# Optimization experiments

Measured on AMD Instinct MI355X. Metric: run time of the kernel, lower is better.

## Reference

```python
import jax, jax.numpy as jnp
import numpy as np

EPS = 1e-8  # torch cosine_similarity eps


def setup_inputs() -> dict:
    key = jax.random.key(0)
    ks = jax.random.split(key, 8)
    B, D = 65536, 1024
    s = lambda fi, fo: (1.0 / np.sqrt(fi))
    return {
        "image_features": jax.random.normal(ks[0], (B, D), jnp.float32),
        "W1": jax.random.normal(ks[1], (D, 512), jnp.float32) * s(D, 512),
        "b1": jnp.zeros((512,), jnp.float32),
        "W2": jax.random.normal(ks[2], (512, 256), jnp.float32) * s(512, 256),
        "b2": jnp.zeros((256,), jnp.float32),
        "W3": jax.random.normal(ks[3], (256, 128), jnp.float32) * s(256, 128),
        "b3": jnp.zeros((128,), jnp.float32),
        "emb": jax.random.normal(ks[4], (1000, 128), jnp.float32),
    }


def reference(image_features, W1, b1, W2, b2, W3, b3, emb):
    # MLP projection (dropout is identity at inference)
    h = jax.nn.relu(image_features @ W1 + b1)
    h = jax.nn.relu(h @ W2 + b2)
    proj = h @ W3 + b3                              # [B, 128]
    # cosine similarity against all 1000 scene embeddings, fused as
    # normalize + small matmul instead of the broadcasted [B,1000,128] tensor
    pn = proj / jnp.maximum(jnp.linalg.norm(proj, axis=-1, keepdims=True), EPS)
    en = emb / jnp.maximum(jnp.linalg.norm(emb, axis=-1, keepdims=True), EPS)
    sims = pn @ en.T                                # [B, 1000]
    top_indices = jnp.argmax(sims, axis=1)          # [B]
    return top_indices
```

## Files before the change

kernel.cpp:

```cpp
#include <hip/hip_runtime.h>
#include <math.h>

#define EPS 1e-8f
#define TAU 1e-4f

typedef _Float16 half_t;
typedef __attribute__((ext_vector_type(8))) _Float16 f16x8;
typedef __attribute__((ext_vector_type(4))) float f32x4;

__device__ __forceinline__ void gload16(const half_t* g, half_t* l) {
    __builtin_amdgcn_global_load_lds((const __attribute__((address_space(1))) void*)g,
                                     (__attribute__((address_space(3))) void*)l, 16, 0, 0);
}

__device__ __forceinline__ void split2(float a, half_t& h, half_t& l) {
    h = (half_t)a;
    l = (half_t)(a - (float)h);
}


__global__ __launch_bounds__(64) void emb_norm_kernel(const float* __restrict__ emb,
                                                      float* __restrict__ enT) {
    const int row = blockIdx.x;
    const int t = threadIdx.x;
    float e0 = emb[row * 128 + t];
    float e1 = emb[row * 128 + 64 + t];
    float s = e0 * e0 + e1 * e1;
#pragma unroll
    for (int off = 32; off >= 1; off >>= 1) s += __shfl_xor(s, off);
    float denom = fmaxf(sqrtf(s), EPS);
    enT[(size_t)t * 1000 + row]        = e0 / denom;
    enT[(size_t)(64 + t) * 1000 + row] = e1 / denom;
}

__global__ __launch_bounds__(64) void emb_split_kernel(const float* __restrict__ emb,
                                                       half_t* __restrict__ eTh,
                                                       half_t* __restrict__ eTl) {
    const int n = blockIdx.x;
    const int t = threadIdx.x;
    float e0 = 0.f, e1 = 0.f;
    if (n < 1000) {
        e0 = emb[n * 128 + t];
        e1 = emb[n * 128 + 64 + t];
    }
    float s = e0 * e0 + e1 * e1;
#pragma unroll
    for (int off = 32; off >= 1; off >>= 1) s += __shfl_xor(s, off);
    float denom = fmaxf(sqrtf(s), EPS);
    float v0 = (n < 1000) ? e0 / denom : 0.f;
    float v1 = (n < 1000) ? e1 / denom : 0.f;
    half_t h, l;
    int f0 = t, f1 = 64 + t;
    size_t p0 = ((size_t)(f0 >> 3) * 1024 + n) * 8 + (f0 & 7);
    size_t p1 = ((size_t)(f1 >> 3) * 1024 + n) * 8 + (f1 & 7);
    split2(v0, h, l); eTh[p0] = h; eTl[p0] = l;
    split2(v1, h, l); eTh[p1] = h; eTl[p1] = l;
}

template<int N>
__global__ __launch_bounds__(256) void wsplit_kernel(const float* __restrict__ W,
                                                     half_t* __restrict__ Wh,
                                                     half_t* __restrict__ Wl) {
    int idx = blockIdx.x * 256 + threadIdx.x;
    int k = idx / N, n = idx % N;
    float w = W[idx];
    half_t h, l;
    split2(w, h, l);
    size_t pos = ((size_t)(k >> 3) * N + n) * 8 + (k & 7);
    Wh[pos] = h; Wl[pos] = l;
}

#define EPI_RELU 0
#define EPI_NORM 1

template<int K, int N, bool AF32, int EPI>
__global__ __launch_bounds__(256, 2) void gemm16(
    const float* __restrict__ A32,
    const half_t* __restrict__ Agh, const half_t* __restrict__ Agl,
    const half_t* __restrict__ Bgh, const half_t* __restrict__ Bgl,
    const float* __restrict__ bias,
    half_t* __restrict__ Oh, half_t* __restrict__ Ol)
{
    __shared__ alignas(16) half_t sAh[8][128][8];
    __shared__ alignas(16) half_t sAl[8][128][8];
    __shared__ alignas(16) half_t sBh[8][128][8];
    __shared__ alignas(16) half_t sBl[8][128][8];

    const int t = threadIdx.x;
    const int lane = t & 63, w = t >> 6;
    const int lr = lane & 15, lg = lane >> 4;
    const int wm = w >> 1, wn = w & 1;

    const int nwg = gridDim.x * gridDim.y;
    const int lin = blockIdx.x + gridDim.x * blockIdx.y;
    const int cpx = nwg >> 3;
    const int logical = (lin & 7) * cpx + (lin >> 3);
    const int bx = logical % gridDim.x;
    const int by = logical / gridDim.x;
    const int m0 = by * 128, n0 = bx * 128;

    f32x4 acc[4][4] = {};

    for (int k0 = 0; k0 < K; k0 += 64) {
        if constexpr (AF32) {
#pragma unroll
            for (int q = 0; q < 4; ++q) {
                int s = t + 256 * q;
                int row = s >> 3, kb = s & 7;
                const float* src = A32 + (size_t)(m0 + row) * K + k0 + kb * 8;
                float4 v0 = *(const float4*)src;
                float4 v1 = *(const float4*)(src + 4);
                float vv[8] = {v0.x, v0.y, v0.z, v0.w, v1.x, v1.y, v1.z, v1.w};
                f16x8 hi, lo;
#pragma unroll
                for (int i = 0; i < 8; ++i) {
                    half_t h = (half_t)vv[i];
                    hi[i] = h;
                    lo[i] = (half_t)(vv[i] - (float)h);
                }
                int prow = row ^ kb;
                *(f16x8*)&sAh[kb][prow][0] = hi;
                *(f16x8*)&sAl[kb][prow][0] = lo;
            }
        } else {
#pragma unroll
            for (int i = 0; i < 4; ++i) {
                int s = (w << 8) + (i << 6) + lane;
                int kb = s >> 7, prow = s & 127;
                int row = prow ^ kb;
                size_t go = (size_t)(m0 + row) * K + k0 + kb * 8;
                gload16(Agh + go, &sAh[0][0][0] + (size_t)s * 8);
                gload16(Agl + go, &sAl[0][0][0] + (size_t)s * 8);
            }
        }
#pragma unroll
        for (int i = 0; i < 4; ++i) {
            int s = (w << 8) + (i << 6) + lane;
            int kb = s >> 7, col = s & 127;
            size_t go = ((size_t)(k0 / 8 + kb) * N + n0 + col) * 8;
            gload16(Bgh + go, &sBh[0][0][0] + (size_t)s * 8);
            gload16(Bgl + go, &sBl[0][0][0] + (size_t)s * 8);
        }
        __syncthreads();
#pragma unroll
        for (int ks = 0; ks < 2; ++ks) {
            const int kb = ks * 4 + lg;
            f16x8 ah[4], al[4], bh[4], bl[4];
#pragma unroll
            for (int mf = 0; mf < 4; ++mf) {
                int row = wm * 64 + mf * 16 + lr;
                int prow = row ^ kb;
                ah[mf] = *(const f16x8*)&sAh[kb][prow][0];
                al[mf] = *(const f16x8*)&sAl[kb][prow][0];
            }
#pragma unroll
            for (int nf = 0; nf < 4; ++nf) {
                int col = wn * 64 + nf * 16 + lr;
                bh[nf] = *(const f16x8*)&sBh[kb][col][0];
                bl[nf] = *(const f16x8*)&sBl[kb][col][0];
            }
#pragma unroll
            for (int mf = 0; mf < 4; ++mf)
#pragma unroll
                for (int nf = 0; nf < 4; ++nf) {
                    acc[mf][nf] = __builtin_amdgcn_mfma_f32_16x16x32_f16(ah[mf], bh[nf], acc[mf][nf], 0, 0, 0);
                    acc[mf][nf] = __builtin_amdgcn_mfma_f32_16x16x32_f16(ah[mf], bl[nf], acc[mf][nf], 0, 0, 0);
                    acc[mf][nf] = __builtin_amdgcn_mfma_f32_16x16x32_f16(al[mf], bh[nf], acc[mf][nf], 0, 0, 0);
                }
        }
        __syncthreads();
    }

    if constexpr (EPI == EPI_RELU) {
#pragma unroll
        for (int nf = 0; nf < 4; ++nf) {
            int n = n0 + wn * 64 + nf * 16 + lr;
            float bb = bias[n];
#pragma unroll
            for (int mf = 0; mf < 4; ++mf)
#pragma unroll
                for (int r = 0; r < 4; ++r) {
                    int m = m0 + wm * 64 + mf * 16 + lg * 4 + r;
                    float v = acc[mf][nf][r] + bb;
                    v = fmaxf(v, 0.f);
                    half_t h, l;
                    split2(v, h, l);
                    Oh[(size_t)m * N + n] = h;
                    Ol[(size_t)m * N + n] = l;
                }
        }
    } else {
        __shared__ float nsum[2][128];
#pragma unroll
        for (int nf = 0; nf < 4; ++nf) {
            float bb = bias[wn * 64 + nf * 16 + lr];
#pragma unroll
            for (int mf = 0; mf < 4; ++mf)
#pragma unroll
                for (int r = 0; r < 4; ++r) acc[mf][nf][r] += bb;
        }
#pragma unroll
        for (int mf = 0; mf < 4; ++mf)
#pragma unroll
            for (int r = 0; r < 4; ++r) {
                float s = 0.f;
#pragma unroll
                for (int nf = 0; nf < 4; ++nf) {
                    float v = acc[mf][nf][r];
                    s += v * v;
                }
#pragma unroll
                for (int off = 1; off < 16; off <<= 1) s += __shfl_xor(s, off);
                if (lr == 0) nsum[wn][wm * 64 + mf * 16 + lg * 4 + r] = s;
            }
        __syncthreads();
#pragma unroll
        for (int mf = 0; mf < 4; ++mf)
#pragma unroll
            for (int r = 0; r < 4; ++r) {
                int ml = wm * 64 + mf * 16 + lg * 4 + r;
                float tot = nsum[0][ml] + nsum[1][ml];
                float sc = 1.0f / fmaxf(sqrtf(tot), EPS);
                int m = m0 + ml;
#pragma unroll
                for (int nf = 0; nf < 4; ++nf) {
                    int n = wn * 64 + nf * 16 + lr;
                    float v = acc[mf][nf][r] * sc;
                    half_t h, l;
                    split2(v, h, l);
                    Oh[(size_t)m * 128 + n] = h;
                    Ol[(size_t)m * 128 + n] = l;
                }
            }
    }
}

__global__ void zero_count_kernel(int* c) { if (threadIdx.x == 0) *c = 0; }

__global__ __launch_bounds__(256, 2) void sims64_kernel(
    const half_t* __restrict__ pnh, const half_t* __restrict__ pnl,
    const half_t* __restrict__ eTh, const half_t* __restrict__ eTl,
    int* __restrict__ out, int* __restrict__ list, int* __restrict__ cnt,
    int Mtot)
{
    __shared__ alignas(16) half_t sPnH[16 * 64 * 8];
    __shared__ alignas(16) half_t sPnL[16 * 64 * 8];
    __shared__ alignas(16) half_t sEH[16 * 64 * 8];
    __shared__ alignas(16) half_t sEL[16 * 64 * 8];
    __shared__ float sv1[128];
    __shared__ int   si1[128];
    __shared__ float sv2[128];

    const int t = threadIdx.x;
    const int lane = t & 63, w = t >> 6;
    const int lr = lane & 15, lg = lane >> 4;
    const int wm = w >> 1, wn = w & 1;
    const int m0 = blockIdx.x * 64;

#pragma unroll
    for (int i = 0; i < 4; ++i) {
        int s = t + 256 * i;
        int kb = s >> 6, row = s & 63;
        size_t go = (size_t)(m0 + row) * 128 + kb * 8;
        gload16(pnh + go, sPnH + (size_t)s * 8);
        gload16(pnl + go, sPnL + (size_t)s * 8);
    }
#pragma unroll
    for (int i = 0; i < 4; ++i) {
        int s = t + 256 * i;
        int kb = s >> 6, col = s & 63;
        size_t go = ((size_t)kb * 1024 + col) * 8;
        gload16(eTh + go, sEH + (size_t)s * 8);
        gload16(eTl + go, sEL + (size_t)s * 8);
    }

    float tv1[2][4], tv2[2][4];
    int ti1[2][4];
#pragma unroll
    for (int mf = 0; mf < 2; ++mf)
#pragma unroll
        for (int r = 0; r < 4; ++r) { tv1[mf][r] = -INFINITY; tv2[mf][r] = -INFINITY; ti1[mf][r] = 0; }

    for (int nt = 0; nt < 16; ++nt) {
        __syncthreads();
        f32x4 acc[2][2] = {};
#pragma unroll
        for (int ks = 0; ks < 4; ++ks) {
            const int kb = ks * 4 + lg;
            f16x8 ah[2], al[2], bh[2], bl[2];
#pragma unroll
            for (int mf = 0; mf < 2; ++mf) {
                int row = wm * 32 + mf * 16 + lr;
                ah[mf] = *(const f16x8*)(sPnH + ((size_t)kb * 64 + row) * 8);
                al[mf] = *(const f16x8*)(sPnL + ((size_t)kb * 64 + row) * 8);
            }
#pragma unroll
            for (int nf = 0; nf < 2; ++nf) {
                int col = wn * 32 + nf * 16 + lr;
                bh[nf] = *(const f16x8*)(sEH + ((size_t)kb * 64 + col) * 8);
                bl[nf] = *(const f16x8*)(sEL + ((size_t)kb * 64 + col) * 8);
            }
#pragma unroll
            for (int mf = 0; mf < 2; ++mf)
#pragma unroll
                for (int nf = 0; nf < 2; ++nf) {
                    acc[mf][nf] = __builtin_amdgcn_mfma_f32_16x16x32_f16(ah[mf], bh[nf], acc[mf][nf], 0, 0, 0);
                    acc[mf][nf] = __builtin_amdgcn_mfma_f32_16x16x32_f16(ah[mf], bl[nf], acc[mf][nf], 0, 0, 0);
                    acc[mf][nf] = __builtin_amdgcn_mfma_f32_16x16x32_f16(al[mf], bh[nf], acc[mf][nf], 0, 0, 0);
                }
        }
#pragma unroll
        for (int mf = 0; mf < 2; ++mf)
#pragma unroll
            for (int nf = 0; nf < 2; ++nf) {
                int gc = nt * 64 + wn * 32 + nf * 16 + lr;
#pragma unroll
                for (int r = 0; r < 4; ++r) {
                    float v = (gc < 1000) ? acc[mf][nf][r] : -INFINITY;
                    if (v > tv1[mf][r]) { tv2[mf][r] = tv1[mf][r]; tv1[mf][r] = v; ti1[mf][r] = gc; }
                    else if (v > tv2[mf][r]) tv2[mf][r] = v;
                }
            }
        __syncthreads();
        if (nt < 15) {
            int ntn = nt + 1;
#pragma unroll
            for (int i = 0; i < 4; ++i) {
                int s = t + 256 * i;
                int kb = s >> 6, col = s & 63;
                size_t go = ((size_t)kb * 1024 + ntn * 64 + col) * 8;
                gload16(eTh + go, sEH + (size_t)s * 8);
                gload16(eTl + go, sEL + (size_t)s * 8);
            }
        }
    }

#pragma unroll
    for (int mf = 0; mf < 2; ++mf)
#pragma unroll
        for (int r = 0; r < 4; ++r) {
            float v1 = tv1[mf][r], v2 = tv2[mf][r];
            int i1 = ti1[mf][r];
#pragma unroll
            for (int off = 1; off < 16; off <<= 1) {
                float ov1 = __shfl_xor(v1, off);
                int   oi1 = __shfl_xor(i1, off);
                float ov2 = __shfl_xor(v2, off);
                if (ov1 > v1) { v2 = fmaxf(v1, ov2); v1 = ov1; i1 = oi1; }
                else if (ov1 == v1) { v2 = fmaxf(v2, ov1); if (oi1 < i1) i1 = oi1; }
                else { v2 = fmaxf(v2, ov1); }
            }
            if (lr == 0) {
                int ml = wm * 32 + mf * 16 + lg * 4 + r;
                sv1[wn * 64 + ml] = v1; si1[wn * 64 + ml] = i1; sv2[wn * 64 + ml] = v2;
            }
        }
    __syncthreads();
    if (t < 64) {
        float v1 = sv1[t]; int i1 = si1[t]; float v2 = sv2[t];
        float ov1 = sv1[64 + t]; int oi1 = si1[64 + t]; float ov2 = sv2[64 + t];
        if (ov1 > v1) { v2 = fmaxf(v1, ov2); v1 = ov1; i1 = oi1; }
        else if (ov1 == v1) { v2 = fmaxf(v2, ov1); if (oi1 < i1) i1 = oi1; }
        else { v2 = fmaxf(v2, ov1); }
        out[m0 + t] = i1;
        if (v1 - v2 < TAU) {
            int p = atomicAdd(cnt, 1);
            if (p < Mtot) list[p] = m0 + t;
        }
    }
}

__global__ __launch_bounds__(256) void recheck_row_kernel(
    const float* __restrict__ img,
    const float* __restrict__ W1, const float* __restrict__ b1,
    const float* __restrict__ W2, const float* __restrict__ b2,
    const float* __restrict__ W3, const float* __restrict__ b3,
    const float* __restrict__ enT,
    const int* __restrict__ list, const int* __restrict__ count,
    int* __restrict__ out, int maxcnt)
{
    __shared__ float sx[1024];
    __shared__ float sh1[512];
    __shared__ float sh2[256];
    __shared__ float sp[128];
    __shared__ float sden;
    __shared__ float redv[4];
    __shared__ int   redi[4];

    const int t = threadIdx.x;
    const int lane = t & 63, wv = t >> 6;
    int cnt = *count;
    if (cnt > maxcnt) cnt = maxcnt;

    for (int b = blockIdx.x; b < cnt; b += gridDim.x) {
        const int row = list[b];
        *(float4*)&sx[t * 4] = *(const float4*)(img + (size_t)row * 1024 + t * 4);
        __syncthreads();
        {
            float a0 = 0.f, a1 = 0.f;
#pragma unroll 8
            for (int k = 0; k < 1024; ++k) {
                float xv = sx[k];
                float2 wv2 = *(const float2*)(W1 + (size_t)k * 512 + 2 * t);
                a0 = fmaf(xv, wv2.x, a0);
                a1 = fmaf(xv, wv2.y, a1);
            }
            sh1[2 * t]     = fmaxf(a0 + b1[2 * t], 0.f);
            sh1[2 * t + 1] = fmaxf(a1 + b1[2 * t + 1], 0.f);
        }
        __syncthreads();
        {
            float a = 0.f;
#pragma unroll 8
            for (int k = 0; k < 512; ++k)
                a = fmaf(sh1[k], W2[(size_t)k * 256 + t], a);
            sh2[t] = fmaxf(a + b2[t], 0.f);
        }
        __syncthreads();
        if (t < 128) {
            float a = 0.f;
#pragma unroll 8
            for (int k = 0; k < 256; ++k)
                a = fmaf(sh2[k], W3[(size_t)k * 128 + t], a);
            sp[t] = a + b3[t];
        }
        __syncthreads();
        if (t < 64) {
            float s = sp[t] * sp[t] + sp[t + 64] * sp[t + 64];
#pragma unroll
            for (int off = 32; off >= 1; off >>= 1) s += __shfl_xor(s, off);
            if (t == 0) sden = fmaxf(sqrtf(s), EPS);
        }
        __syncthreads();
        if (t < 128) sp[t] = sp[t] / sden;
        __syncthreads();
        float bm = -INFINITY;
        int bi = 0;
#pragma unroll
        for (int j = 0; j < 4; ++j) {
            const int c = t + 256 * j;
            if (c < 1000) {
                float a = 0.f;
#pragma unroll 8
                for (int k = 0; k < 128; ++k)
                    a = fmaf(sp[k], enT[(size_t)k * 1000 + c], a);
                if (a > bm) { bm = a; bi = c; }
            }
        }
#pragma unroll
        for (int off = 1; off < 64; off <<= 1) {
            float om = __shfl_xor(bm, off);
            int oi = __shfl_xor(bi, off);
            if (om > bm || (om == bm && oi < bi)) { bm = om; bi = oi; }
        }
        if (lane == 0) { redv[wv] = bm; redi[wv] = bi; }
        __syncthreads();
        if (t == 0) {
            float v = redv[0]; int i = redi[0];
#pragma unroll
            for (int q = 1; q < 4; ++q) {
                if (redv[q] > v || (redv[q] == v && redi[q] < i)) { v = redv[q]; i = redi[q]; }
            }
            out[row] = i;
        }
        __syncthreads();
    }
}

__global__ __launch_bounds__(256) void scene_exact_kernel(
    const float* __restrict__ img,
    const float* __restrict__ W1, const float* __restrict__ b1,
    const float* __restrict__ W2, const float* __restrict__ b2,
    const float* __restrict__ W3, const float* __restrict__ b3,
    const float* __restrict__ enT,
    int* __restrict__ out)
{
    __shared__ float sImg[16][64];
    __shared__ float sH1[16][512];
    __shared__ float sH2[16][256];
    __shared__ float sPn[16][128];

    const int tid = threadIdx.x;
    const int base = blockIdx.x * 16;

    {
        const int tx = tid & 63, ty = tid >> 6;
        float acc[4][8] = {};
        for (int k0 = 0; k0 < 1024; k0 += 64) {
            {
                const int r = tid >> 4, c4 = tid & 15;
                float4 v = *(const float4*)(img + (size_t)(base + r) * 1024 + k0 + c4 * 4);
                *(float4*)(&sImg[r][c4 * 4]) = v;
            }
            __syncthreads();
#pragma unroll 4
            for (int kk = 0; kk < 64; ++kk) {
                const int k = k0 + kk;
                float a[4];
#pragma unroll
                for (int i = 0; i < 4; ++i) a[i] = sImg[ty + 4 * i][kk];
#pragma unroll
                for (int j = 0; j < 8; ++j) {
                    float wv = W1[(size_t)k * 512 + tx + 64 * j];
#pragma unroll
                    for (int i = 0; i < 4; ++i) acc[i][j] = fmaf(a[i], wv, acc[i][j]);
                }
            }
            __syncthreads();
        }
#pragma unroll
        for (int j = 0; j < 8; ++j) {
            float bb = b1[tx + 64 * j];
#pragma unroll
            for (int i = 0; i < 4; ++i) {
                float v = acc[i][j] + bb;
                sH1[ty + 4 * i][tx + 64 * j] = v > 0.f ? v : 0.f;
            }
        }
        __syncthreads();
    }
    {
        const int tx = tid & 63, ty = tid >> 6;
        float acc[4][4] = {};
#pragma unroll 4
        for (int k = 0; k < 512; ++k) {
            float a[4];
#pragma unroll
            for (int i = 0; i < 4; ++i) a[i] = sH1[ty + 4 * i][k];
#pragma unroll
            for (int j = 0; j < 4; ++j) {
                float wv = W2[(size_t)k * 256 + tx + 64 * j];
#pragma unroll
                for (int i = 0; i < 4; ++i) acc[i][j] = fmaf(a[i], wv, acc[i][j]);
            }
        }
        __syncthreads();
#pragma unroll
        for (int j = 0; j < 4; ++j) {
            float bb = b2[tx + 64 * j];
#pragma unroll
            for (int i = 0; i < 4; ++i) {
                float v = acc[i][j] + bb;
                sH2[ty + 4 * i][tx + 64 * j] = v > 0.f ? v : 0.f;
            }
        }
        __syncthreads();
    }
    {
        const int tx = tid & 31, ty = tid >> 5;
        float acc[2][4] = {};
#pragma unroll 4
        for (int k = 0; k < 256; ++k) {
            float a[2];
#pragma unroll
            for (int i = 0; i < 2; ++i) a[i] = sH2[ty + 8 * i][k];
#pragma unroll
            for (int j = 0; j < 4; ++j) {
                float wv = W3[(size_t)k * 128 + tx + 32 * j];
#pragma unroll
                for (int i = 0; i < 2; ++i) acc[i][j] = fmaf(a[i], wv, acc[i][j]);
            }
        }
#pragma unroll
        for (int j = 0; j < 4; ++j) {
            float bb = b3[tx + 32 * j];
#pragma unroll
            for (int i = 0; i < 2; ++i) sPn[ty + 8 * i][tx + 32 * j] = acc[i][j] + bb;
        }
        __syncthreads();
    }
    {
        const int r = tid >> 4, sub = tid & 15;
        float s = 0.f;
#pragma unroll
        for (int m = 0; m < 8; ++m) {
            float v = sPn[r][sub + 16 * m];
            s += v * v;
        }
#pragma unroll
        for (int off = 1; off < 16; off <<= 1) s += __shfl_xor(s, off);
        float denom = fmaxf(sqrtf(s), EPS);
#pragma unroll
        for (int m = 0; m < 8; ++m) sPn[r][sub + 16 * m] /= denom;
        __syncthreads();
    }
    {
        const int ct = tid & 63, rg = tid >> 6;
        float bm[4]; int bi[4];
#pragma unroll
        for (int i = 0; i < 4; ++i) { bm[i] = -INFINITY; bi[i] = 0; }
#pragma unroll
        for (int tpass = 0; tpass < 2; ++tpass) {
            const int tt = ct + 64 * tpass;
            if (tt < 125) {
                const int c0 = tt * 8;
                float acc[4][8] = {};
#pragma unroll 4
                for (int k = 0; k < 128; ++k) {
                    float p[4];
#pragma unroll
                    for (int i = 0; i < 4; ++i) p[i] = sPn[rg * 4 + i][k];
                    const float* ep = enT + (size_t)k * 1000 + c0;
                    float4 e0 = *(const float4*)(ep);
                    float4 e1 = *(const float4*)(ep + 4);
                    float e[8] = {e0.x, e0.y, e0.z, e0.w, e1.x, e1.y, e1.z, e1.w};
#pragma unroll
                    for (int j = 0; j < 8; ++j)
#pragma unroll
                        for (int i = 0; i < 4; ++i) acc[i][j] = fmaf(p[i], e[j], acc[i][j]);
                }
#pragma unroll
                for (int j = 0; j < 8; ++j) {
                    const int c = c0 + j;
#pragma unroll
                    for (int i = 0; i < 4; ++i)
                        if (acc[i][j] > bm[i]) { bm[i] = acc[i][j]; bi[i] = c; }
                }
            }
        }
#pragma unroll
        for (int off = 1; off < 64; off <<= 1) {
#pragma unroll
            for (int i = 0; i < 4; ++i) {
                float om = __shfl_xor(bm[i], off);
                int oi = __shfl_xor(bi[i], off);
                if (om > bm[i] || (om == bm[i] && oi < bi[i])) { bm[i] = om; bi[i] = oi; }
            }
        }
        if (ct == 0) {
#pragma unroll
            for (int i = 0; i < 4; ++i) out[base + rg * 4 + i] = bi[i];
        }
    }
}

extern "C" void kernel_launch(void* const* d_in, const int* in_sizes, int n_in,
                              void* d_out, int out_size, void* d_ws, size_t ws_size,
                              hipStream_t stream) {
    const float* img = (const float*)d_in[0];
    const float* W1  = (const float*)d_in[1];
    const float* b1  = (const float*)d_in[2];
    const float* W2  = (const float*)d_in[3];
    const float* b2  = (const float*)d_in[4];
    const float* W3  = (const float*)d_in[5];
    const float* b3  = (const float*)d_in[6];
    const float* emb = (const float*)d_in[7];
    int* out = (int*)d_out;
    const int B = in_sizes[0] / 1024;

    size_t off = 0;
    auto carve = [&](size_t bytes) {
        void* p = (char*)d_ws + off;
        off += (bytes + 255) & ~(size_t)255;
        return p;
    };
    float*  enT  = (float*)carve(128 * 1000 * 4);
    half_t* W1h  = (half_t*)carve((size_t)1024 * 512 * 2);
    half_t* W1l  = (half_t*)carve((size_t)1024 * 512 * 2);
    half_t* W2h  = (half_t*)carve((size_t)512 * 256 * 2);
    half_t* W2l  = (half_t*)carve((size_t)512 * 256 * 2);
    half_t* W3h  = (half_t*)carve((size_t)256 * 128 * 2);
    half_t* W3l  = (half_t*)carve((size_t)256 * 128 * 2);
    half_t* eTh  = (half_t*)carve((size_t)16 * 1024 * 8 * 2);
    half_t* eTl  = (half_t*)carve((size_t)16 * 1024 * 8 * 2);
    half_t* h1h  = (half_t*)carve((size_t)B * 512 * 2);
    half_t* h1l  = (half_t*)carve((size_t)B * 512 * 2);
    half_t* h2h  = (half_t*)carve((size_t)B * 256 * 2);
    half_t* h2l  = (half_t*)carve((size_t)B * 256 * 2);
    const size_t REQUIRE = off;

    if (ws_size < REQUIRE) {
        emb_norm_kernel<<<1000, 64, 0, stream>>>(emb, (float*)d_ws);
        scene_exact_kernel<<<B / 16, 256, 0, stream>>>(
            img, W1, b1, W2, b2, W3, b3, (float*)d_ws, out);
        return;
    }

    half_t* pnh  = h1h;
    half_t* pnl  = (half_t*)((char*)h1h + (size_t)B * 128 * 2);
    int*    list = (int*)((char*)h1h + (size_t)B * 128 * 4);
    int*    cnt  = (int*)((char*)list + (size_t)B * 4);

    emb_norm_kernel<<<1000, 64, 0, stream>>>(emb, enT);
    emb_split_kernel<<<1024, 64, 0, stream>>>(emb, eTh, eTl);
    wsplit_kernel<512><<<(1024 * 512) / 256, 256, 0, stream>>>(W1, W1h, W1l);
    wsplit_kernel<256><<<(512 * 256) / 256, 256, 0, stream>>>(W2, W2h, W2l);
    wsplit_kernel<128><<<(256 * 128) / 256, 256, 0, stream>>>(W3, W3h, W3l);

    gemm16<1024, 512, true, EPI_RELU><<<dim3(4, B / 128), 256, 0, stream>>>(
        img, nullptr, nullptr, W1h, W1l, b1, h1h, h1l);
    gemm16<512, 256, false, EPI_RELU><<<dim3(2, B / 128), 256, 0, stream>>>(
        nullptr, h1h, h1l, W2h, W2l, b2, h2h, h2l);
    gemm16<256, 128, false, EPI_NORM><<<dim3(1, B / 128), 256, 0, stream>>>(
        nullptr, h2h, h2l, W3h, W3l, b3, pnh, pnl);

    zero_count_kernel<<<1, 64, 0, stream>>>(cnt);
    sims64_kernel<<<B / 64, 256, 0, stream>>>(
        pnh, pnl, eTh, eTl, out, list, cnt, B);

    recheck_row_kernel<<<2048, 256, 0, stream>>>(
        img, W1, b1, W2, b2, W3, b3, enT, list, cnt, out, B);
}
```

Baseline: 568.6 us.

## Merge prep kernels into one launch and halve GEMM K-tile for occupancy

Folds the five small preprocessing launches (embedding normalisation, embedding split, three weight splits) into a single block-partitioned prep kernel, which removes launch overhead. The split-fp16 GEMM now uses a K-step of 32 instead of 64, halving its LDS footprint, and launch bounds request 4 waves per SIMD instead of 2 so more workgroups can be resident. The cost is twice as many K iterations and barriers per tile, and a tighter register budget that may cause spills with the 4x4 accumulator tile.

```diff
diff --git a/kernel.cpp b/kernel.cpp
--- a/kernel.cpp
+++ b/kernel.cpp
@@ -18,6 +18,69 @@
     l = (half_t)(a - (float)h);
 }
 
+__global__ __launch_bounds__(256) void prep_kernel(
+    const float* __restrict__ emb, float* __restrict__ enT,
+    half_t* __restrict__ eTh, half_t* __restrict__ eTl,
+    const float* __restrict__ W1, half_t* __restrict__ W1h, half_t* __restrict__ W1l,
+    const float* __restrict__ W2, half_t* __restrict__ W2h, half_t* __restrict__ W2l,
+    const float* __restrict__ W3, half_t* __restrict__ W3h, half_t* __restrict__ W3l)
+{
+    const int b = blockIdx.x;
+    const int t = threadIdx.x;
+    if (b < 250) {
+        const int row = b * 4 + (t >> 6);
+        const int lane = t & 63;
+        float e0 = emb[row * 128 + lane];
+        float e1 = emb[row * 128 + 64 + lane];
+        float s = e0 * e0 + e1 * e1;
+#pragma unroll
+        for (int off = 32; off >= 1; off >>= 1) s += __shfl_xor(s, off);
+        float denom = fmaxf(sqrtf(s), EPS);
+        enT[(size_t)lane * 1000 + row]        = e0 / denom;
+        enT[(size_t)(64 + lane) * 1000 + row] = e1 / denom;
+    } else if (b < 506) {
+        const int n = (b - 250) * 4 + (t >> 6);
+        const int lane = t & 63;
+        float e0 = 0.f, e1 = 0.f;
+        if (n < 1000) {
+            e0 = emb[n * 128 + lane];
+            e1 = emb[n * 128 + 64 + lane];
+        }
+        float s = e0 * e0 + e1 * e1;
+#pragma unroll
+        for (int off = 32; off >= 1; off >>= 1) s += __shfl_xor(s, off);
+        float denom = fmaxf(sqrtf(s), EPS);
+        float v0 = (n < 1000) ? e0 / denom : 0.f;
+        float v1 = (n < 1000) ? e1 / denom : 0.f;
+        half_t h, l;
+        int f0 = lane, f1 = 64 + lane;
+        size_t p0 = ((size_t)(f0 >> 3) * 1024 + n) * 8 + (f0 & 7);
+        size_t p1 = ((size_t)(f1 >> 3) * 1024 + n) * 8 + (f1 & 7);
+        split2(v0, h, l); eTh[p0] = h; eTl[p0] = l;
+        split2(v1, h, l); eTh[p1] = h; eTl[p1] = l;
+    } else if (b < 2554) {
+        int idx = (b - 506) * 256 + t;
+        int k = idx / 512, n = idx % 512;
+        half_t h, l;
+        split2(W1[idx], h, l);
+        size_t pos = ((size_t)(k >> 3) * 512 + n) * 8 + (k & 7);
+        W1h[pos] = h; W1l[pos] = l;
+    } else if (b < 3066) {
+        int idx = (b - 2554) * 256 + t;
+        int k = idx / 256, n = idx % 256;
+        half_t h, l;
+        split2(W2[idx], h, l);
+        size_t pos = ((size_t)(k >> 3) * 256 + n) * 8 + (k & 7);
+        W2h[pos] = h; W2l[pos] = l;
+    } else {
+        int idx = (b - 3066) * 256 + t;
+        int k = idx / 128, n = idx % 128;
+        half_t h, l;
+        split2(W3[idx], h, l);
+        size_t pos = ((size_t)(k >> 3) * 128 + n) * 8 + (k & 7);
+        W3h[pos] = h; W3l[pos] = l;
+    }
+}
 
 __global__ __launch_bounds__(64) void emb_norm_kernel(const float* __restrict__ emb,
                                                       float* __restrict__ enT) {
@@ -33,58 +96,21 @@
     enT[(size_t)(64 + t) * 1000 + row] = e1 / denom;
 }
 
-__global__ __launch_bounds__(64) void emb_split_kernel(const float* __restrict__ emb,
-                                                       half_t* __restrict__ eTh,
-                                                       half_t* __restrict__ eTl) {
-    const int n = blockIdx.x;
-    const int t = threadIdx.x;
-    float e0 = 0.f, e1 = 0.f;
-    if (n < 1000) {
-        e0 = emb[n * 128 + t];
-        e1 = emb[n * 128 + 64 + t];
-    }
-    float s = e0 * e0 + e1 * e1;
-#pragma unroll
-    for (int off = 32; off >= 1; off >>= 1) s += __shfl_xor(s, off);
-    float denom = fmaxf(sqrtf(s), EPS);
-    float v0 = (n < 1000) ? e0 / denom : 0.f;
-    float v1 = (n < 1000) ? e1 / denom : 0.f;
-    half_t h, l;
-    int f0 = t, f1 = 64 + t;
-    size_t p0 = ((size_t)(f0 >> 3) * 1024 + n) * 8 + (f0 & 7);
-    size_t p1 = ((size_t)(f1 >> 3) * 1024 + n) * 8 + (f1 & 7);
-    split2(v0, h, l); eTh[p0] = h; eTl[p0] = l;
-    split2(v1, h, l); eTh[p1] = h; eTl[p1] = l;
-}
-
-template<int N>
-__global__ __launch_bounds__(256) void wsplit_kernel(const float* __restrict__ W,
-                                                     half_t* __restrict__ Wh,
-                                                     half_t* __restrict__ Wl) {
-    int idx = blockIdx.x * 256 + threadIdx.x;
-    int k = idx / N, n = idx % N;
-    float w = W[idx];
-    half_t h, l;
-    split2(w, h, l);
-    size_t pos = ((size_t)(k >> 3) * N + n) * 8 + (k & 7);
-    Wh[pos] = h; Wl[pos] = l;
-}
-
 #define EPI_RELU 0
 #define EPI_NORM 1
 
 template<int K, int N, bool AF32, int EPI>
-__global__ __launch_bounds__(256, 2) void gemm16(
+__global__ __launch_bounds__(256, 4) void gemm16(
     const float* __restrict__ A32,
     const half_t* __restrict__ Agh, const half_t* __restrict__ Agl,
     const half_t* __restrict__ Bgh, const half_t* __restrict__ Bgl,
     const float* __restrict__ bias,
     half_t* __restrict__ Oh, half_t* __restrict__ Ol)
 {
-    __shared__ alignas(16) half_t sAh[8][128][8];
-    __shared__ alignas(16) half_t sAl[8][128][8];
-    __shared__ alignas(16) half_t sBh[8][128][8];
-    __shared__ alignas(16) half_t sBl[8][128][8];
+    __shared__ alignas(16) half_t sAh[4][128][8];
+    __shared__ alignas(16) half_t sAl[4][128][8];
+    __shared__ alignas(16) half_t sBh[4][128][8];
+    __shared__ alignas(16) half_t sBl[4][128][8];
 
     const int t = threadIdx.x;
     const int lane = t & 63, w = t >> 6;
@@ -101,12 +127,12 @@
 
     f32x4 acc[4][4] = {};
 
-    for (int k0 = 0; k0 < K; k0 += 64) {
+    for (int k0 = 0; k0 < K; k0 += 32) {
         if constexpr (AF32) {
 #pragma unroll
-            for (int q = 0; q < 4; ++q) {
+            for (int q = 0; q < 2; ++q) {
                 int s = t + 256 * q;
-                int row = s >> 3, kb = s & 7;
+                int row = s >> 2, kb = s & 3;
                 const float* src = A32 + (size_t)(m0 + row) * K + k0 + kb * 8;
                 float4 v0 = *(const float4*)src;
                 float4 v1 = *(const float4*)(src + 4);
@@ -124,8 +150,8 @@
             }
         } else {
 #pragma unroll
-            for (int i = 0; i < 4; ++i) {
-                int s = (w << 8) + (i << 6) + lane;
+            for (int i = 0; i < 2; ++i) {
+                int s = (w << 7) + (i << 6) + lane;
                 int kb = s >> 7, prow = s & 127;
                 int row = prow ^ kb;
                 size_t go = (size_t)(m0 + row) * K + k0 + kb * 8;
@@ -134,17 +160,16 @@
             }
         }
 #pragma unroll
-        for (int i = 0; i < 4; ++i) {
-            int s = (w << 8) + (i << 6) + lane;
+        for (int i = 0; i < 2; ++i) {
+            int s = (w << 7) + (i << 6) + lane;
             int kb = s >> 7, col = s & 127;
             size_t go = ((size_t)(k0 / 8 + kb) * N + n0 + col) * 8;
             gload16(Bgh + go, &sBh[0][0][0] + (size_t)s * 8);
             gload16(Bgl + go, &sBl[0][0][0] + (size_t)s * 8);
         }
         __syncthreads();
-#pragma unroll
-        for (int ks = 0; ks < 2; ++ks) {
-            const int kb = ks * 4 + lg;
+        {
+            const int kb = lg;
             f16x8 ah[4], al[4], bh[4], bl[4];
 #pragma unroll
             for (int mf = 0; mf < 4; ++mf) {
@@ -681,11 +706,8 @@
     int*    list = (int*)((char*)h1h + (size_t)B * 128 * 4);
     int*    cnt  = (int*)((char*)list + (size_t)B * 4);
 
-    emb_norm_kernel<<<1000, 64, 0, stream>>>(emb, enT);
-    emb_split_kernel<<<1024, 64, 0, stream>>>(emb, eTh, eTl);
-    wsplit_kernel<512><<<(1024 * 512) / 256, 256, 0, stream>>>(W1, W1h, W1l);
-    wsplit_kernel<256><<<(512 * 256) / 256, 256, 0, stream>>>(W2, W2h, W2l);
-    wsplit_kernel<128><<<(256 * 128) / 256, 256, 0, stream>>>(W3, W3h, W3l);
+    prep_kernel<<<3194, 256, 0, stream>>>(emb, enT, eTh, eTl,
+                                          W1, W1h, W1l, W2, W2h, W2l, W3, W3h, W3l);
 
     gemm16<1024, 512, true, EPI_RELU><<<dim3(4, B / 128), 256, 0, stream>>>(
         img, nullptr, nullptr, W1h, W1l, b1, h1h, h1l);
```

Result: slower. 719.7 us (+26.6%).
